# Optimization experiments

Measured on AMD Instinct MI355X. Metric: run time of the kernel, lower is better.

Reference implementation:

```python
import jax, jax.numpy as jnp
import numpy as np

RES = 64

TRI_TABLE = jnp.array([
    [-1,-1,-1,-1,-1,-1],[1,0,2,-1,-1,-1],[4,0,3,-1,-1,-1],[1,4,2,1,3,4],
    [3,1,5,-1,-1,-1],[2,3,0,2,5,3],[1,4,0,1,5,4],[4,2,5,-1,-1,-1],
    [4,5,2,-1,-1,-1],[4,1,0,4,5,1],[3,2,0,3,5,2],[1,3,5,-1,-1,-1],
    [4,1,2,4,3,1],[3,0,4,-1,-1,-1],[2,0,1,-1,-1,-1],[-1,-1,-1,-1,-1,-1]], dtype=jnp.int32)
NUM_TRI = jnp.array([0,1,1,2,1,2,2,1,1,2,2,1,2,1,1,0], dtype=jnp.int32)
BASE_EDGES = jnp.array([0,1,0,2,0,3,1,2,1,3,2,3], dtype=jnp.int32)


def _make_tet_grid(res):
    # Kuhn 6-tet decomposition of each cube of a (res+1)^3 grid.
    n = res + 1
    ii, jj, kk = np.meshgrid(np.arange(n), np.arange(n), np.arange(n), indexing='ij')
    verts = (np.stack([ii, jj, kk], -1).reshape(-1, 3).astype(np.float32)) / res
    def vid(i, j, k):
        return (i * n + j) * n + k
    i, j, k = np.meshgrid(np.arange(res), np.arange(res), np.arange(res), indexing='ij')
    i, j, k = i.ravel(), j.ravel(), k.ravel()
    c = [vid(i + (b & 1), j + ((b >> 1) & 1), k + ((b >> 2) & 1)) for b in range(8)]
    kuhn = [(0,1,3,7),(0,3,2,7),(0,2,6,7),(0,6,4,7),(0,4,5,7),(0,5,1,7)]
    tets = np.stack([np.stack([c[a], c[b], c[d], c[e]], -1) for (a, b, d, e) in kuhn], 1)
    return verts, tets.reshape(-1, 4).astype(np.int64)


def setup_inputs() -> dict:
    key = jax.random.key(0)
    verts, tets = _make_tet_grid(RES)
    level = jax.random.normal(key, (verts.shape[0], 1), dtype=jnp.float32)
    return {"level": level, "pos": jnp.asarray(verts), "tet": jnp.asarray(tets), "threshold": 0}


def reference(level, pos, tet, threshold):
    sdf = level - threshold                    # [N,1]
    occ = sdf[:, 0] > 0                        # [N]
    occ_fx4 = occ[tet]                         # [F,4]
    occ_sum = occ_fx4.sum(-1)
    valid = (occ_sum > 0) & (occ_sum < 4)
    vt = tet[valid]                            # [Fv,4]
    occ_valid = occ_fx4[valid]                 # [Fv,4]

    edges = jnp.sort(vt[:, BASE_EDGES].reshape(-1, 2), axis=1)   # [Fv*6,2]
    unique_edges, idx_map = jnp.unique(edges, axis=0, return_inverse=True)
    idx_map = idx_map.reshape(-1)
    mask_edges = occ[unique_edges].sum(-1) == 1                  # crossing edges
    mapping = jnp.where(mask_edges, jnp.cumsum(mask_edges) - 1, -1)
    idx_map = mapping[idx_map].reshape(-1, 6)                    # [Fv,6]
    interp_v = unique_edges[mask_edges]                          # [M,2]

    p = pos[interp_v]                                            # [M,2,3]
    s = sdf[interp_v][..., 0] * jnp.array([1.0, -1.0], dtype=sdf.dtype)  # [M,2]
    w = s[:, ::-1] / s.sum(1, keepdims=True)                     # flip / denom
    verts_out = (p * w[..., None]).sum(1)                        # [M,3]

    v_id = 2 ** jnp.arange(4, dtype=jnp.int32)
    tetindex = (occ_valid.astype(jnp.int32) * v_id).sum(-1)      # [Fv]
    num_tri = NUM_TRI[tetindex]
    m1, m2 = num_tri == 1, num_tri == 2
    f1 = jnp.take_along_axis(idx_map[m1], TRI_TABLE[tetindex[m1]][:, :3], axis=1).reshape(-1, 3)
    f2 = jnp.take_along_axis(idx_map[m2], TRI_TABLE[tetindex[m2]][:, :6], axis=1).reshape(-1, 3)
    faces = jnp.concatenate([f1, f2], axis=0)
    return verts_out, faces
```

## Files before the change

kernel.cpp:

```cpp
#include <hip/hip_runtime.h>


#define RESX 64
#define NV   65
#define NV2  4225
#define NVERT 274625
#define NCUBE 262144
#define BLOCK 256
#define NGRP 1073
#define CGRP 1024
#define NBLK1 269
#define CBLK 1024
#define WINW 20
#define STAGE 9216
#define M21 0x1fffffu

__constant__ int c_tri[16][6] = {
    {-1,-1,-1,-1,-1,-1},{1,0,2,-1,-1,-1},{4,0,3,-1,-1,-1},{1,4,2,1,3,4},
    {3,1,5,-1,-1,-1},{2,3,0,2,5,3},{1,4,0,1,5,4},{4,2,5,-1,-1,-1},
    {4,5,2,-1,-1,-1},{4,1,0,4,5,1},{3,2,0,3,5,2},{1,3,5,-1,-1,-1},
    {4,1,2,4,3,1},{3,0,4,-1,-1,-1},{2,0,1,-1,-1,-1},{-1,-1,-1,-1,-1,-1}};
__constant__ int c_ntri[16] = {0,1,1,2,1,2,2,1,1,2,2,1,2,1,1,0};
__constant__ int c_kuhn[6][4] = {{0,1,3,7},{0,3,2,7},{0,2,6,7},{0,6,4,7},{0,4,5,7},{0,5,1,7}};
__constant__ int c_off8[8] = {0,4225,65,4290,1,4226,66,4291};
__constant__ int c_loc[6][6] = {
    {0,0,0,1,1,3},{0,0,0,2,3,2},{0,0,0,2,2,6},
    {0,0,0,4,6,4},{0,0,0,4,4,5},{0,0,0,1,5,1}};
__constant__ int c_dir[6][6] = {
    {3,5,6,1,2,0},{5,1,6,3,0,4},{1,2,6,0,4,3},
    {2,0,6,1,3,5},{0,4,6,3,5,1},{4,3,6,0,1,2}};

typedef unsigned long long u64;
#define NTRI_PACK 0x16696994u

__device__ __forceinline__ u64 block_reduce_u64(u64 v, u64* lds) {
    int tid = threadIdx.x, lane = tid & 63, w = tid >> 6;
#pragma unroll
    for (int off = 32; off > 0; off >>= 1)
        v += __shfl_xor(v, off, 64);
    if (lane == 0) lds[w] = v;
    __syncthreads();
    if (tid == 0) lds[4] = lds[0] + lds[1] + lds[2] + lds[3];
    __syncthreads();
    return lds[4];
}

__device__ __forceinline__ unsigned block_scan_excl(unsigned val, unsigned* lds,
                                                    unsigned& block_total) {
    int tid = threadIdx.x, lane = tid & 63, w = tid >> 6;
    unsigned x = val;
#pragma unroll
    for (int off = 1; off < 64; off <<= 1) {
        unsigned y = (unsigned)__shfl_up((int)x, off, 64);
        if (lane >= off) x += y;
    }
    if (lane == 63) lds[w] = x;
    __syncthreads();
    if (tid == 0) {
        unsigned s = 0;
#pragma unroll
        for (int i = 0; i < 4; i++) { unsigned t = lds[i]; lds[i + 4] = s; s += t; }
        lds[8] = s;
    }
    __syncthreads();
    block_total = lds[8];
    return x - val + lds[4 + w];
}

__global__ void __launch_bounds__(256)
pass1(const float* __restrict__ level, const float* __restrict__ thrp,
      unsigned char* __restrict__ flagsArr, unsigned short* __restrict__ locEx,
      u64* __restrict__ bsAll) {
    int tid = threadIdx.x, lane = tid & 63, w = tid >> 6;
    int group = blockIdx.x * 4 + w;
    if (group >= NGRP) return;
    float thr = thrp[0];

    int v = group * 256 + lane * 4;
    unsigned fl[4] = {0, 0, 0, 0};
    if (v <= NVERT - 4295) {
        float r0[5], rY[5], rX[5], rXY[5];
#pragma unroll
        for (int e = 0; e < 5; e++) {
            r0[e]  = level[v + e]        - thr;
            rY[e]  = level[v + 65 + e]   - thr;
            rX[e]  = level[v + 4225 + e] - thr;
            rXY[e] = level[v + 4290 + e] - thr;
        }
        int i0 = v / NV2; int r = v - i0 * NV2; int j0 = r / NV; int k0 = r - j0 * NV;
#pragma unroll
        for (int d = 0; d < 4; d++) {
            int kk = k0 + d, jj = j0;
            if (kk > 64) { kk -= 65; jj += 1; }
            if (jj > 64) { jj -= 65; }
            bool oky = jj < RESX, okz = kk < RESX;
            bool s0 = r0[d] > 0.f;
            unsigned f = s0 ? 0x80u : 0u;
            if (okz &&        ((r0[d+1]  > 0.f) != s0)) f |= 1u;
            if (oky &&        ((rY[d]    > 0.f) != s0)) f |= 2u;
            if (oky && okz && ((rY[d+1]  > 0.f) != s0)) f |= 4u;
            if (              ((rX[d]    > 0.f) != s0)) f |= 8u;
            if (okz &&        ((rX[d+1]  > 0.f) != s0)) f |= 16u;
            if (oky &&        ((rXY[d]   > 0.f) != s0)) f |= 32u;
            if (oky && okz && ((rXY[d+1] > 0.f) != s0)) f |= 64u;
            fl[d] = f;
        }
    } else {
        const int b2d[8] = {0, 3, 1, 5, 0, 4, 2, 6};
#pragma unroll
        for (int d = 0; d < 4; d++) {
            int g = v + d;
            if (g >= NVERT) continue;
            int i = g / NV2; int r = g - i * NV2; int j = r / NV; int k = r - j * NV;
            bool okx = i < RESX, oky = j < RESX, okz = k < RESX;
            float s = level[g] - thr;
            bool s0 = s > 0.f;
            unsigned f = s0 ? 0x80u : 0u;
#pragma unroll
            for (int b = 1; b < 8; b++) {
                bool ok = (!(b & 1) || okx) && (!(b & 2) || oky) && (!(b & 4) || okz);
                if (ok) {
                    float vb = level[g + c_off8[b]] - thr;
                    if ((vb > 0.f) != s0) f |= (1u << b2d[b]);
                }
            }
            fl[d] = f;
        }
    }
    unsigned cnt[4];
#pragma unroll
    for (int d = 0; d < 4; d++) cnt[d] = __popc(fl[d] & 0x7fu);
    unsigned cth = cnt[0] + cnt[1] + cnt[2] + cnt[3];
    unsigned x = cth;
#pragma unroll
    for (int off = 1; off < 64; off <<= 1) {
        unsigned y = (unsigned)__shfl_up((int)x, off, 64);
        if (lane >= off) x += y;
    }
    unsigned wex = x - cth;
    unsigned totE = (unsigned)__shfl((int)x, 63, 64);
    if (v + 3 < NVERT) {
        *(uchar4*)(flagsArr + v) = make_uchar4((unsigned char)fl[0], (unsigned char)fl[1],
                                               (unsigned char)fl[2], (unsigned char)fl[3]);
        ushort4 e4;
        e4.x = (unsigned short)wex;
        e4.y = (unsigned short)(wex + cnt[0]);
        e4.z = (unsigned short)(wex + cnt[0] + cnt[1]);
        e4.w = (unsigned short)(wex + cnt[0] + cnt[1] + cnt[2]);
        *(ushort4*)(locEx + v) = e4;
    } else {
        unsigned e = wex;
        for (int d = 0; d < 4; d++) {
            int g = v + d;
            if (g < NVERT) {
                flagsArr[g] = (unsigned char)fl[d];
                locEx[g] = (unsigned short)e;
                e += cnt[d];
            }
        }
    }

    unsigned c1 = 0, c2 = 0;
    if (group < CGRP) {
        int c0 = group * 256 + lane * 4;
        int ci = c0 >> 12, cj = (c0 >> 6) & 63, ck = c0 & 63;
        int base = (ci * NV + cj) * NV + ck;
        float q0[5], qY[5], qX[5], qXY[5];
#pragma unroll
        for (int e = 0; e < 5; e++) {
            q0[e]  = level[base + e]        - thr;
            qY[e]  = level[base + 65 + e]   - thr;
            qX[e]  = level[base + 4225 + e] - thr;
            qXY[e] = level[base + 4290 + e] - thr;
        }
#pragma unroll
        for (int d = 0; d < 4; d++) {
            unsigned occ8 = (q0[d]   > 0.f ?   1u : 0u) | (qX[d]   > 0.f ?   2u : 0u)
                          | (qY[d]   > 0.f ?   4u : 0u) | (qXY[d]  > 0.f ?   8u : 0u)
                          | (q0[d+1] > 0.f ?  16u : 0u) | (qX[d+1] > 0.f ?  32u : 0u)
                          | (qY[d+1] > 0.f ?  64u : 0u) | (qXY[d+1]> 0.f ? 128u : 0u);
#pragma unroll
            for (int t = 0; t < 6; t++) {
                int cfg = ((occ8 >> c_kuhn[t][0]) & 1) | (((occ8 >> c_kuhn[t][1]) & 1) << 1)
                        | (((occ8 >> c_kuhn[t][2]) & 1) << 2) | (((occ8 >> c_kuhn[t][3]) & 1) << 3);
                unsigned nt = (NTRI_PACK >> (cfg << 1)) & 3u;
                c1 += (nt == 1);
                c2 += (nt == 2);
            }
        }
        unsigned pk = c1 | (c2 << 16);
#pragma unroll
        for (int off = 32; off; off >>= 1) pk += (unsigned)__shfl_xor((int)pk, off, 64);
        c1 = pk & 0xffffu; c2 = pk >> 16;
    }
    if (lane == 0)
        bsAll[group] = (u64)totE | ((u64)c1 << 16) | ((u64)c2 << 32);
}

__global__ void __launch_bounds__(256)
pass2(const float* __restrict__ level, const float* __restrict__ thrp,
      const unsigned char* __restrict__ flagsArr,
      const unsigned short* __restrict__ locEx,
      const u64* __restrict__ bsAll, float* __restrict__ out) {
    __shared__ unsigned lds[9];
    __shared__ u64 lds64[5];
    __shared__ unsigned win[WINW];
    __shared__ unsigned pEw[WINW];
    __shared__ float stage[STAGE];
    int tid = threadIdx.x;
    int bid = blockIdx.x;
    int gid = bid * BLOCK + tid;
    float thr = thrp[0];

    int g0 = bid << 8;
    int wci = g0 >> 12, wcj = (g0 >> 6) & 63;
    int wb = (bid < CBLK) ? (((wci * NV + wcj) * NV) >> 8) : 0;

    unsigned lE = 0, lEp = 0, lWb = 0, l1 = 0, l1p = 0, l2p = 0;
    for (int t = tid; t < NGRP; t += BLOCK) {
        u64 a = bsAll[t];
        unsigned e  = (unsigned)a & 0xffffu;
        unsigned x1 = (unsigned)(a >> 16) & 0xffffu;
        unsigned x2 = (unsigned)(a >> 32) & 0xffffu;
        lE += e; l1 += x1;
        if (t < bid) { lEp += e; l1p += x1; l2p += x2; }
        if (t < wb)  { lWb += e; }
    }
    if (tid < WINW) {
        int t = wb + tid;
        win[tid] = (t < NGRP) ? ((unsigned)bsAll[t] & 0xffffu) : 0u;
    }
    float cv[8];
    {
        int gsafe = (gid < NVERT) ? gid : 0;
#pragma unroll
        for (int b = 0; b < 8; b++) {
            int a = gsafe + c_off8[b];
            cv[b] = level[a < NVERT ? a : 0] - thr;
        }
    }
    u64 r0 = block_reduce_u64((u64)lE | ((u64)lEp << 21) | ((u64)lWb << 42), lds64);
    u64 r1 = block_reduce_u64((u64)l1 | ((u64)l1p << 21) | ((u64)l2p << 42), lds64);
    unsigned M    = (unsigned)r0 & M21;
    unsigned pE   = (unsigned)(r0 >> 21) & M21;
    unsigned wAcc = (unsigned)(r0 >> 42);
    unsigned C1   = (unsigned)r1 & M21;
    unsigned p1b  = (unsigned)(r1 >> 21) & M21;
    unsigned p2b  = (unsigned)(r1 >> 42);
    if (tid < WINW) {
        unsigned s = wAcc;
        for (int d = 0; d < tid; d++) s += win[d];
        pEw[tid] = s;
    }

    unsigned totE = (unsigned)bsAll[bid] & 0xffffu;
    if (gid < NVERT) {
        unsigned fl = flagsArr[gid];
        if (fl & 0x7fu) {
            int i = gid / NV2; int r = gid - i * NV2; int j = r / NV; int k = r - j * NV;
            float v0 = cv[0];
            unsigned slot = locEx[gid];
            const float inv = 1.f / 64.f;
            const int d2b[7] = {4, 2, 6, 1, 5, 3, 7};
            float fi = (float)i, fj = (float)j, fk = (float)k;
#pragma unroll
            for (int d = 0; d < 7; d++) {
                if (fl & (1u << d)) {
                    const int b = d2b[d];
                    float s1 = cv[b];
                    float w1 = v0 * __builtin_amdgcn_rcpf(v0 - s1);
                    float* o = &stage[3u * slot];
                    o[0] = (fi + (float)(b & 1) * w1) * inv;
                    o[1] = (fj + (float)((b >> 1) & 1) * w1) * inv;
                    o[2] = (fk + (float)((b >> 2) & 1) * w1) * inv;
                    slot++;
                }
            }
        }
    }
    __syncthreads();
    {
        float* dst = out + 3u * pE;
        unsigned n = totE * 3u;
        for (unsigned idx = tid; idx < n; idx += BLOCK)
            __builtin_nontemporal_store(stage[idx], &dst[idx]);
    }

    if (bid >= CBLK) return;
    __syncthreads();

    int ci = gid >> 12, cj = (gid >> 6) & 63, ck = gid & 63;
    int base = (ci * NV + cj) * NV + ck;
    u64 f8 = 0ull;
#pragma unroll
    for (int b = 0; b < 8; b++)
        f8 |= (u64)flagsArr[base + c_off8[b]] << (8 * b);
    unsigned occ8 = 0;
#pragma unroll
    for (int b = 0; b < 8; b++) occ8 |= (unsigned)((f8 >> (8 * b + 7)) & 1ull) << b;
    int cfgs[6], nts[6];
    unsigned c1 = 0, c2 = 0;
#pragma unroll
    for (int t = 0; t < 6; t++) {
        int cfg = ((occ8 >> c_kuhn[t][0]) & 1) | (((occ8 >> c_kuhn[t][1]) & 1) << 1)
                | (((occ8 >> c_kuhn[t][2]) & 1) << 2) | (((occ8 >> c_kuhn[t][3]) & 1) << 3);
        cfgs[t] = cfg;
        int nt = c_ntri[cfg];
        nts[t] = nt;
        c1 += (nt == 1); c2 += (nt == 2);
    }
    unsigned tot2;
    unsigned ex2 = block_scan_excl(c1 | (c2 << 16), lds, tot2);
    unsigned f1 = tot2 & 0xffffu;
    unsigned f2 = tot2 >> 16;
    unsigned l1c = ex2 & 0xffffu;
    unsigned l2c = ex2 >> 16;
    unsigned n1 = f1 * 3u;
#pragma unroll
    for (int t = 0; t < 6; t++) {
        int nt = nts[t];
        if (nt == 0) continue;
        int cfg = cfgs[t];
        unsigned basef = (nt == 1) ? (3u * l1c) : (n1 + 6u * l2c);
        int cntm = 3 * nt;
        for (int m = 0; m < cntm; m++) {
            int e = c_tri[cfg][m];
            int lc = c_loc[t][e];
            int dir = c_dir[t][e];
            int lo = base + c_off8[lc];
            unsigned flb = (unsigned)((f8 >> (8 * lc)) & 0xffull);
            unsigned rnk = pEw[(lo >> 8) - wb] + locEx[lo]
                         + __popc(flb & ((1u << dir) - 1u));
            stage[basef + (unsigned)m] = (float)rnk;
        }
        l1c += (nt == 1);
        l2c += (nt == 2);
    }
    __syncthreads();
    float* of = out + 3ull * M;
    float* o1 = of + 3u * p1b;
    for (unsigned idx = tid; idx < n1; idx += BLOCK)
        __builtin_nontemporal_store(stage[idx], &o1[idx]);
    unsigned n2 = f2 * 6u;
    float* o2 = of + 3u * (C1 + 2u * p2b);
    for (unsigned idx = tid; idx < n2; idx += BLOCK)
        __builtin_nontemporal_store(stage[n1 + idx], &o2[idx]);
}

extern "C" void kernel_launch(void* const* d_in, const int* in_sizes, int n_in,
                              void* d_out, int out_size, void* d_ws, size_t ws_size,
                              hipStream_t stream) {
    const float* level = (const float*)d_in[0];
    const float* thrp = (const float*)d_in[3];
    float* out = (float*)d_out;

    char* p = (char*)d_ws;
    unsigned char* flagsArr = (unsigned char*)p;
    p += (NVERT + 255) & ~255;
    unsigned short* locEx = (unsigned short*)p;
    p += ((sizeof(unsigned short) * NVERT) + 255) & ~255;
    u64* bsAll = (u64*)p;

    pass1<<<NBLK1, BLOCK, 0, stream>>>(level, thrp, flagsArr, locEx, bsAll);
    pass2<<<NGRP, BLOCK, 0, stream>>>(level, thrp, flagsArr, locEx, bsAll, out);
}
```

Before: 115.7 us.

## Split pass2 into separate vertex and face kernels with half-cube-per-thread face work

Splits the combined vertex/face output kernel into two kernels. The vertex kernel now only computes its own prefix over edge counts. The face kernel runs 2048 blocks with two threads per cube, each handling three tets. Pass1 now emits half-wave triangle counts in separate arrays, so the face kernel's block granularity matches those counts. The aim is smaller LDS stage buffers and higher occupancy (launch bounds 8), plus more parallelism for the serial per-tet face loop. The cost is an extra kernel launch and the face kernel repeating the global prefix reductions over the block summaries.

Measured after the change: 124.3 us. +7.5%, slower.

```diff
diff --git a/kernel.cpp b/kernel.cpp
--- a/kernel.cpp
+++ b/kernel.cpp
@@ -10,9 +10,10 @@
 #define NGRP 1073
 #define CGRP 1024
 #define NBLK1 269
-#define CBLK 1024
+#define FBLK 2048
 #define WINW 20
-#define STAGE 9216
+#define VSTAGE 5376
+#define FSTAGE 4608
 #define M21 0x1fffffu
 
 __constant__ int c_tri[16][6] = {
@@ -70,7 +71,7 @@
 __global__ void __launch_bounds__(256)
 pass1(const float* __restrict__ level, const float* __restrict__ thrp,
       unsigned char* __restrict__ flagsArr, unsigned short* __restrict__ locEx,
-      u64* __restrict__ bsAll) {
+      unsigned* __restrict__ bsE, unsigned* __restrict__ bsT2) {
     int tid = threadIdx.x, lane = tid & 63, w = tid >> 6;
     int group = blockIdx.x * 4 + w;
     if (group >= NGRP) return;
@@ -160,7 +161,7 @@
         }
     }
 
-    unsigned c1 = 0, c2 = 0;
+    unsigned pk = 0;
     if (group < CGRP) {
         int c0 = group * 256 + lane * 4;
         int ci = c0 >> 12, cj = (c0 >> 6) & 63, ck = c0 & 63;
@@ -173,6 +174,7 @@
             qX[e]  = level[base + 4225 + e] - thr;
             qXY[e] = level[base + 4290 + e] - thr;
         }
+        unsigned c1 = 0, c2 = 0;
 #pragma unroll
         for (int d = 0; d < 4; d++) {
             unsigned occ8 = (q0[d]   > 0.f ?   1u : 0u) | (qX[d]   > 0.f ?   2u : 0u)
@@ -188,48 +190,35 @@
                 c2 += (nt == 2);
             }
         }
-        unsigned pk = c1 | (c2 << 16);
-#pragma unroll
-        for (int off = 32; off; off >>= 1) pk += (unsigned)__shfl_xor((int)pk, off, 64);
-        c1 = pk & 0xffffu; c2 = pk >> 16;
-    }
-    if (lane == 0)
-        bsAll[group] = (u64)totE | ((u64)c1 << 16) | ((u64)c2 << 32);
-}
-
-__global__ void __launch_bounds__(256)
-pass2(const float* __restrict__ level, const float* __restrict__ thrp,
-      const unsigned char* __restrict__ flagsArr,
-      const unsigned short* __restrict__ locEx,
-      const u64* __restrict__ bsAll, float* __restrict__ out) {
-    __shared__ unsigned lds[9];
+        pk = c1 | (c2 << 16);
+#pragma unroll
+        for (int off = 16; off; off >>= 1)
+            pk += (unsigned)__shfl_xor((int)pk, off, 64);
+    }
+    unsigned pkB = (unsigned)__shfl((int)pk, 32, 64);
+    if (lane == 0) {
+        bsE[group] = totE;
+        if (group < CGRP) {
+            bsT2[2 * group]     = pk;
+            bsT2[2 * group + 1] = pkB;
+        }
+    }
+}
+
+__global__ void __launch_bounds__(256, 8)
+pass2v(const float* __restrict__ level, const float* __restrict__ thrp,
+       const unsigned char* __restrict__ flagsArr,
+       const unsigned short* __restrict__ locEx,
+       const unsigned* __restrict__ bsE, float* __restrict__ out) {
     __shared__ u64 lds64[5];
-    __shared__ unsigned win[WINW];
-    __shared__ unsigned pEw[WINW];
-    __shared__ float stage[STAGE];
+    __shared__ float stage[VSTAGE];
     int tid = threadIdx.x;
     int bid = blockIdx.x;
     int gid = bid * BLOCK + tid;
     float thr = thrp[0];
 
-    int g0 = bid << 8;
-    int wci = g0 >> 12, wcj = (g0 >> 6) & 63;
-    int wb = (bid < CBLK) ? (((wci * NV + wcj) * NV) >> 8) : 0;
-
-    unsigned lE = 0, lEp = 0, lWb = 0, l1 = 0, l1p = 0, l2p = 0;
-    for (int t = tid; t < NGRP; t += BLOCK) {
-        u64 a = bsAll[t];
-        unsigned e  = (unsigned)a & 0xffffu;
-        unsigned x1 = (unsigned)(a >> 16) & 0xffffu;
-        unsigned x2 = (unsigned)(a >> 32) & 0xffffu;
-        lE += e; l1 += x1;
-        if (t < bid) { lEp += e; l1p += x1; l2p += x2; }
-        if (t < wb)  { lWb += e; }
-    }
-    if (tid < WINW) {
-        int t = wb + tid;
-        win[tid] = (t < NGRP) ? ((unsigned)bsAll[t] & 0xffffu) : 0u;
-    }
+    unsigned lEp = 0;
+    for (int t = tid; t < bid; t += BLOCK) lEp += bsE[t];
     float cv[8];
     {
         int gsafe = (gid < NVERT) ? gid : 0;
@@ -239,21 +228,8 @@
             cv[b] = level[a < NVERT ? a : 0] - thr;
         }
     }
-    u64 r0 = block_reduce_u64((u64)lE | ((u64)lEp << 21) | ((u64)lWb << 42), lds64);
-    u64 r1 = block_reduce_u64((u64)l1 | ((u64)l1p << 21) | ((u64)l2p << 42), lds64);
-    unsigned M    = (unsigned)r0 & M21;
-    unsigned pE   = (unsigned)(r0 >> 21) & M21;
-    unsigned wAcc = (unsigned)(r0 >> 42);
-    unsigned C1   = (unsigned)r1 & M21;
-    unsigned p1b  = (unsigned)(r1 >> 21) & M21;
-    unsigned p2b  = (unsigned)(r1 >> 42);
-    if (tid < WINW) {
-        unsigned s = wAcc;
-        for (int d = 0; d < tid; d++) s += win[d];
-        pEw[tid] = s;
-    }
-
-    unsigned totE = (unsigned)bsAll[bid] & 0xffffu;
+    unsigned pE = (unsigned)block_reduce_u64((u64)lEp, lds64);
+
     if (gid < NVERT) {
         unsigned fl = flagsArr[gid];
         if (fl & 0x7fu) {
@@ -279,17 +255,62 @@
         }
     }
     __syncthreads();
-    {
-        float* dst = out + 3u * pE;
-        unsigned n = totE * 3u;
-        for (unsigned idx = tid; idx < n; idx += BLOCK)
-            __builtin_nontemporal_store(stage[idx], &dst[idx]);
-    }
-
-    if (bid >= CBLK) return;
-    __syncthreads();
-
-    int ci = gid >> 12, cj = (gid >> 6) & 63, ck = gid & 63;
+    unsigned totE = bsE[bid];
+    float* dst = out + 3u * pE;
+    unsigned n = totE * 3u;
+    for (unsigned idx = tid; idx < n; idx += BLOCK)
+        __builtin_nontemporal_store(stage[idx], &dst[idx]);
+}
+
+__global__ void __launch_bounds__(256, 8)
+pass2f(const unsigned char* __restrict__ flagsArr,
+       const unsigned short* __restrict__ locEx,
+       const unsigned* __restrict__ bsE, const unsigned* __restrict__ bsT2,
+       float* __restrict__ out) {
+    __shared__ unsigned lds[9];
+    __shared__ u64 lds64[5];
+    __shared__ unsigned win[WINW];
+    __shared__ unsigned pEw[WINW];
+    __shared__ float stage[FSTAGE];
+    int tid = threadIdx.x;
+    int bid = blockIdx.x;
+    int g0 = bid << 7;
+    int cube = g0 + (tid >> 1);
+    int h = tid & 1;
+
+    int wci = g0 >> 12, wcj = (g0 >> 6) & 63;
+    int wb = ((wci * NV + wcj) * NV) >> 8;
+
+    unsigned lE = 0, lWb = 0;
+    for (int t = tid; t < NGRP; t += BLOCK) {
+        unsigned e = bsE[t];
+        lE += e;
+        if (t < wb) lWb += e;
+    }
+    unsigned l1 = 0, l1p = 0, l2p = 0;
+    for (int t = tid; t < FBLK; t += BLOCK) {
+        unsigned c = bsT2[t];
+        l1 += c & 0xffffu;
+        if (t < bid) { l1p += c & 0xffffu; l2p += c >> 16; }
+    }
+    if (tid < WINW) {
+        int t = wb + tid;
+        win[tid] = (t < NGRP) ? bsE[t] : 0u;
+    }
+    u64 r0 = block_reduce_u64((u64)lE | ((u64)lWb << 21), lds64);
+    u64 r1 = block_reduce_u64((u64)l1 | ((u64)l1p << 21) | ((u64)l2p << 42), lds64);
+    unsigned M    = (unsigned)r0 & M21;
+    unsigned wAcc = (unsigned)(r0 >> 21) & M21;
+    unsigned C1   = (unsigned)r1 & M21;
+    unsigned p1b  = (unsigned)(r1 >> 21) & M21;
+    unsigned p2b  = (unsigned)(r1 >> 42);
+    if (tid < WINW) {
+        unsigned s = wAcc;
+        for (int d = 0; d < tid; d++) s += win[d];
+        pEw[tid] = s;
+    }
+
+    int ci = cube >> 12, cj = (cube >> 6) & 63, ck = cube & 63;
     int base = (ci * NV + cj) * NV + ck;
     u64 f8 = 0ull;
 #pragma unroll
@@ -298,15 +319,16 @@
     unsigned occ8 = 0;
 #pragma unroll
     for (int b = 0; b < 8; b++) occ8 |= (unsigned)((f8 >> (8 * b + 7)) & 1ull) << b;
-    int cfgs[6], nts[6];
+    int cfgs[3], nts[3];
     unsigned c1 = 0, c2 = 0;
 #pragma unroll
-    for (int t = 0; t < 6; t++) {
+    for (int m = 0; m < 3; m++) {
+        int t = h * 3 + m;
         int cfg = ((occ8 >> c_kuhn[t][0]) & 1) | (((occ8 >> c_kuhn[t][1]) & 1) << 1)
                 | (((occ8 >> c_kuhn[t][2]) & 1) << 2) | (((occ8 >> c_kuhn[t][3]) & 1) << 3);
-        cfgs[t] = cfg;
+        cfgs[m] = cfg;
         int nt = c_ntri[cfg];
-        nts[t] = nt;
+        nts[m] = nt;
         c1 += (nt == 1); c2 += (nt == 2);
     }
     unsigned tot2;
@@ -317,21 +339,22 @@
     unsigned l2c = ex2 >> 16;
     unsigned n1 = f1 * 3u;
 #pragma unroll
-    for (int t = 0; t < 6; t++) {
-        int nt = nts[t];
+    for (int m = 0; m < 3; m++) {
+        int nt = nts[m];
         if (nt == 0) continue;
-        int cfg = cfgs[t];
+        int t = h * 3 + m;
+        int cfg = cfgs[m];
         unsigned basef = (nt == 1) ? (3u * l1c) : (n1 + 6u * l2c);
         int cntm = 3 * nt;
-        for (int m = 0; m < cntm; m++) {
-            int e = c_tri[cfg][m];
+        for (int q = 0; q < cntm; q++) {
+            int e = c_tri[cfg][q];
             int lc = c_loc[t][e];
             int dir = c_dir[t][e];
             int lo = base + c_off8[lc];
             unsigned flb = (unsigned)((f8 >> (8 * lc)) & 0xffull);
             unsigned rnk = pEw[(lo >> 8) - wb] + locEx[lo]
                          + __popc(flb & ((1u << dir) - 1u));
-            stage[basef + (unsigned)m] = (float)rnk;
+            stage[basef + (unsigned)q] = (float)rnk;
         }
         l1c += (nt == 1);
         l2c += (nt == 2);
@@ -359,8 +382,10 @@
     p += (NVERT + 255) & ~255;
     unsigned short* locEx = (unsigned short*)p;
     p += ((sizeof(unsigned short) * NVERT) + 255) & ~255;
-    u64* bsAll = (u64*)p;
-
-    pass1<<<NBLK1, BLOCK, 0, stream>>>(level, thrp, flagsArr, locEx, bsAll);
-    pass2<<<NGRP, BLOCK, 0, stream>>>(level, thrp, flagsArr, locEx, bsAll, out);
-}
+    unsigned* bsE = (unsigned*)p;  p += sizeof(unsigned) * NGRP;
+    unsigned* bsT2 = (unsigned*)p;
+
+    pass1<<<NBLK1, BLOCK, 0, stream>>>(level, thrp, flagsArr, locEx, bsE, bsT2);
+    pass2v<<<NGRP, BLOCK, 0, stream>>>(level, thrp, flagsArr, locEx, bsE, out);
+    pass2f<<<FBLK, BLOCK, 0, stream>>>(flagsArr, locEx, bsE, bsT2, out);
+}
```
